# Performance work log

Measured on AMD Instinct MI355X. Metric: run time of the kernel, lower is better.

Reference implementation:

```python
import jax, jax.numpy as jnp
import numpy as np

B, N = 64, 32768

def setup_inputs() -> dict:
    key = jax.random.key(0)
    k1, k2, k3, k4 = jax.random.split(key, 4)
    audio = jax.random.normal(k1, (B, N), dtype=jnp.float32)
    g = jax.random.uniform(k2, (B, N, 1), dtype=jnp.float32)
    twoR = jax.random.uniform(k3, (B, N, 1), dtype=jnp.float32)
    mix = jax.random.uniform(k4, (B, N, 3), dtype=jnp.float32)
    return {"audio": audio, "g": g, "twoR": twoR, "mix": mix}


def _svf(audio, g, twoR, mix):
    b, n = audio.shape
    T = 1.0 / (1.0 + g * (g + twoR))                      # [B,N,1]
    ones = jnp.ones_like(g)
    # H: [B,N,2,2] time-varying state matrix
    H = T[..., None] * jnp.concatenate(
        [ones, -g, g, twoR * g + 1.0], axis=-1).reshape(b, n, 2, 2)
    gHB = (g * T) * jnp.concatenate([ones, g], axis=-1)   # [B,N,2]
    gHBx = gHB * audio[..., None]                          # [B,N,2]

    # Linear time-varying recurrence: Y_t = gHBx_t + H_t @ s_{t-1}; s_t = 2 Y_t - s_{t-1}
    def step(state, inp):
        Ht, ut = inp                                       # [B,2,2], [B,2]
        Yt = ut + jnp.einsum('bij,bj->bi', Ht, state)
        return 2.0 * Yt - state, Yt

    s0 = jnp.ones((b, 2), dtype=audio.dtype)
    _, Y = jax.lax.scan(step,
                        s0,
                        (jnp.moveaxis(H, 1, 0), jnp.moveaxis(gHBx, 1, 0)))
    Y = jnp.moveaxis(Y, 0, 1)                              # [B,N,2]

    twoR_ = twoR[..., 0]                                   # [B,N]
    y_bp, y_lp = Y[..., 0], Y[..., 1]
    y_hp = audio - twoR_ * y_bp - y_lp
    y_mixed = twoR_ * mix[..., 0] * y_bp + mix[..., 1] * y_lp + mix[..., 2] * y_hp
    return y_mixed


def reference(audio, g, twoR, mix):
    return _svf(audio, g, twoR, mix)
```

## Files before the change

### kernel.cpp

```cpp
#include <hip/hip_runtime.h>


#define BATCH     64
#define SEQ       32768
#define CHUNKS    16
#define CHUNK_LEN (SEQ / CHUNKS)
#define TPB       256
#define STEPS     (CHUNK_LEN / TPB)
#define NBLK      (BATCH * CHUNKS)

struct Aff { float a00, a01, a10, a11, b0, b1; };

__device__ __forceinline__ Aff compose(const Aff l, const Aff e) {
    Aff r;
    r.a00 = fmaf(l.a00, e.a00, l.a01 * e.a10);
    r.a01 = fmaf(l.a00, e.a01, l.a01 * e.a11);
    r.a10 = fmaf(l.a10, e.a00, l.a11 * e.a10);
    r.a11 = fmaf(l.a10, e.a01, l.a11 * e.a11);
    r.b0  = fmaf(l.a00, e.b0, fmaf(l.a01, e.b1, l.b0));
    r.b1  = fmaf(l.a10, e.b0, fmaf(l.a11, e.b1, l.b1));
    return r;
}

__device__ __forceinline__ Aff step_affine(float gi, float Ri, float xi) {
    float T  = 1.0f / fmaf(gi, gi + Ri, 1.0f);
    float Tg = T * gi;
    Aff r;
    r.a00 = 2.0f * T - 1.0f;
    r.a01 = -2.0f * Tg;
    r.a10 = 2.0f * Tg;
    r.a11 = 2.0f * fmaf(Tg, Ri, T) - 1.0f;
    r.b0  = 2.0f * Tg * xi;
    r.b1  = gi * r.b0;
    return r;
}

__device__ __forceinline__ Aff block_scan_incl(Aff v, Aff (*buf)[TPB], int t) {
    int src = 0;
    buf[0][t] = v;
    __syncthreads();
#pragma unroll
    for (int off = 1; off < TPB; off <<= 1) {
        Aff cur = buf[src][t];
        int idx = (t >= off) ? (t - off) : 0;
        Aff prev = buf[src][idx];
        Aff res = (t >= off) ? compose(cur, prev) : cur;
        buf[1 - src][t] = res;
        src ^= 1;
        __syncthreads();
    }
    return buf[src][t];
}

__device__ __forceinline__ void load8(const float* __restrict__ p, int base, float v[8]) {
    float4 a = *reinterpret_cast<const float4*>(p + base);
    float4 b = *reinterpret_cast<const float4*>(p + base + 4);
    v[0]=a.x; v[1]=a.y; v[2]=a.z; v[3]=a.w; v[4]=b.x; v[5]=b.y; v[6]=b.z; v[7]=b.w;
}

__global__ __launch_bounds__(TPB) void svf_chunk_reduce(
    const float* __restrict__ audio, const float* __restrict__ g,
    const float* __restrict__ twoR, Aff* __restrict__ chunk_comp)
{
    __shared__ Aff buf[2][TPB];
    const int t    = threadIdx.x;
    const int base = blockIdx.x * CHUNK_LEN + t * STEPS;

    float gv[STEPS], rv[STEPS], xv[STEPS];
    load8(g, base, gv); load8(twoR, base, rv); load8(audio, base, xv);

    Aff acc = step_affine(gv[0], rv[0], xv[0]);
#pragma unroll
    for (int i = 1; i < STEPS; ++i)
        acc = compose(step_affine(gv[i], rv[i], xv[i]), acc);

    Aff tot = block_scan_incl(acc, buf, t);
    if (t == TPB - 1) chunk_comp[blockIdx.x] = tot;
}

__global__ __launch_bounds__(TPB) void svf_emit(
    const float* __restrict__ audio, const float* __restrict__ g,
    const float* __restrict__ twoR, const float* __restrict__ mix,
    const Aff* __restrict__ chunk_comp, float* __restrict__ out)
{
    __shared__ Aff buf[2][TPB];
    const int blk  = blockIdx.x;
    const int b    = blk / CHUNKS;
    const int t    = threadIdx.x;
    const int base = blk * CHUNK_LEN + t * STEPS;

    float gv[STEPS], rv[STEPS], xv[STEPS];
    load8(g, base, gv); load8(twoR, base, rv); load8(audio, base, xv);

    Aff acc = step_affine(gv[0], rv[0], xv[0]);
#pragma unroll
    for (int i = 1; i < STEPS; ++i)
        acc = compose(step_affine(gv[i], rv[i], xv[i]), acc);

    Aff incl = block_scan_incl(acc, buf, t);
    buf[0][t] = incl;
    __syncthreads();

    float cs0 = 1.0f, cs1 = 1.0f;
    for (int cc = b * CHUNKS; cc < blk; ++cc) {
        Aff a = chunk_comp[cc];
        float n0 = fmaf(a.a00, cs0, fmaf(a.a01, cs1, a.b0));
        float n1 = fmaf(a.a10, cs0, fmaf(a.a11, cs1, a.b1));
        cs0 = n0; cs1 = n1;
    }

    float s0, s1;
    if (t == 0) { s0 = cs0; s1 = cs1; }
    else {
        Aff p = buf[0][t - 1];
        s0 = fmaf(p.a00, cs0, fmaf(p.a01, cs1, p.b0));
        s1 = fmaf(p.a10, cs0, fmaf(p.a11, cs1, p.b1));
    }

    const float4* m4 = reinterpret_cast<const float4*>(mix + 3 * base);
    float mv[24];
#pragma unroll
    for (int q = 0; q < 6; ++q) {
        float4 m = m4[q];
        mv[4*q+0]=m.x; mv[4*q+1]=m.y; mv[4*q+2]=m.z; mv[4*q+3]=m.w;
    }

    float ov[STEPS];
#pragma unroll
    for (int i = 0; i < STEPS; ++i) {
        float gi = gv[i], Ri = rv[i], xi = xv[i];
        float T  = 1.0f / fmaf(gi, gi + Ri, 1.0f);
        float w  = fmaf(gi, xi, s0);
        float Y0 = T * fmaf(-gi, s1, w);
        float Y1 = T * fmaf(gi, w, fmaf(Ri, gi, 1.0f) * s1);
        float hp = xi - Ri * Y0 - Y1;
        ov[i] = fmaf(Ri * mv[3*i], Y0, fmaf(mv[3*i+1], Y1, mv[3*i+2] * hp));
        s0 = fmaf(2.0f, Y0, -s0);
        s1 = fmaf(2.0f, Y1, -s1);
    }

    *reinterpret_cast<float4*>(out + base)     = make_float4(ov[0], ov[1], ov[2], ov[3]);
    *reinterpret_cast<float4*>(out + base + 4) = make_float4(ov[4], ov[5], ov[6], ov[7]);
}

extern "C" void kernel_launch(void* const* d_in, const int* in_sizes, int n_in,
                              void* d_out, int out_size, void* d_ws, size_t ws_size,
                              hipStream_t stream) {
    const float* audio = (const float*)d_in[0];
    const float* g     = (const float*)d_in[1];
    const float* twoR  = (const float*)d_in[2];
    const float* mix   = (const float*)d_in[3];
    float* out = (float*)d_out;
    Aff* chunk_comp = (Aff*)d_ws;

    svf_chunk_reduce<<<NBLK, TPB, 0, stream>>>(audio, g, twoR, chunk_comp);
    svf_emit<<<NBLK, TPB, 0, stream>>>(audio, g, twoR, mix, chunk_comp, out);
}
```

Baseline: 95.58 us.

## Fuse two-pass chunked scan into single kernel with decoupled flag-based chunk handoff

Merges the chunk-reduce and emit kernels into one kernel. Each block publishes its chunk affine composite through a global flag with release semantics, and later chunks spin on the flags of their predecessors. This removes the second full read of g, twoR and audio and one kernel launch. It adds a memset per call and relies on forward progress of earlier block indices for the spin-wait, which risks deadlock if blocks are not scheduled in order.

Result: slower. 157.4 us (+64.6%).

```diff
diff --git a/kernel.cpp b/kernel.cpp
--- a/kernel.cpp
+++ b/kernel.cpp
@@ -58,34 +58,19 @@
     v[0]=a.x; v[1]=a.y; v[2]=a.z; v[3]=a.w; v[4]=b.x; v[5]=b.y; v[6]=b.z; v[7]=b.w;
 }
 
-__global__ __launch_bounds__(TPB) void svf_chunk_reduce(
+__global__ __launch_bounds__(TPB, 4) void svf_fused(
     const float* __restrict__ audio, const float* __restrict__ g,
-    const float* __restrict__ twoR, Aff* __restrict__ chunk_comp)
+    const float* __restrict__ twoR, const float* __restrict__ mix,
+    float* __restrict__ out,
+    unsigned int* __restrict__ flags, Aff* __restrict__ chunk_aff)
 {
     __shared__ Aff buf[2][TPB];
-    const int t    = threadIdx.x;
-    const int base = blockIdx.x * CHUNK_LEN + t * STEPS;
+    __shared__ float pred[CHUNKS - 1][6];
+    __shared__ float cs_sh[2];
 
-    float gv[STEPS], rv[STEPS], xv[STEPS];
-    load8(g, base, gv); load8(twoR, base, rv); load8(audio, base, xv);
-
-    Aff acc = step_affine(gv[0], rv[0], xv[0]);
-#pragma unroll
-    for (int i = 1; i < STEPS; ++i)
-        acc = compose(step_affine(gv[i], rv[i], xv[i]), acc);
-
-    Aff tot = block_scan_incl(acc, buf, t);
-    if (t == TPB - 1) chunk_comp[blockIdx.x] = tot;
-}
-
-__global__ __launch_bounds__(TPB) void svf_emit(
-    const float* __restrict__ audio, const float* __restrict__ g,
-    const float* __restrict__ twoR, const float* __restrict__ mix,
-    const Aff* __restrict__ chunk_comp, float* __restrict__ out)
-{
-    __shared__ Aff buf[2][TPB];
     const int blk  = blockIdx.x;
-    const int b    = blk / CHUNKS;
+    const int b    = blk >> 4;
+    const int c    = blk & (CHUNKS - 1);
     const int t    = threadIdx.x;
     const int base = blk * CHUNK_LEN + t * STEPS;
 
@@ -97,17 +82,46 @@
     for (int i = 1; i < STEPS; ++i)
         acc = compose(step_affine(gv[i], rv[i], xv[i]), acc);
 
+    const float4* m4 = reinterpret_cast<const float4*>(mix + 3 * base);
+    float mv[24];
+#pragma unroll
+    for (int q = 0; q < 6; ++q) {
+        float4 m = m4[q];
+        mv[4*q+0]=m.x; mv[4*q+1]=m.y; mv[4*q+2]=m.z; mv[4*q+3]=m.w;
+    }
+
     Aff incl = block_scan_incl(acc, buf, t);
-    buf[0][t] = incl;
+
+    if (t == TPB - 1 && c < CHUNKS - 1) {
+        chunk_aff[blk] = incl;
+        __threadfence();
+        __hip_atomic_store(&flags[blk], 1u, __ATOMIC_RELEASE, __HIP_MEMORY_SCOPE_AGENT);
+    }
+
+    if (t < c) {
+        const int cc = b * CHUNKS + t;
+        while (__hip_atomic_load(&flags[cc], __ATOMIC_ACQUIRE,
+                                 __HIP_MEMORY_SCOPE_AGENT) == 0u) {
+            __builtin_amdgcn_s_sleep(1);
+        }
+        Aff a = chunk_aff[cc];
+        pred[t][0] = a.a00; pred[t][1] = a.a01; pred[t][2] = a.a10;
+        pred[t][3] = a.a11; pred[t][4] = a.b0;  pred[t][5] = a.b1;
+    }
     __syncthreads();
 
-    float cs0 = 1.0f, cs1 = 1.0f;
-    for (int cc = b * CHUNKS; cc < blk; ++cc) {
-        Aff a = chunk_comp[cc];
-        float n0 = fmaf(a.a00, cs0, fmaf(a.a01, cs1, a.b0));
-        float n1 = fmaf(a.a10, cs0, fmaf(a.a11, cs1, a.b1));
-        cs0 = n0; cs1 = n1;
+    if (t == 0) {
+        float s0 = 1.0f, s1 = 1.0f;
+        for (int j = 0; j < c; ++j) {
+            float n0 = fmaf(pred[j][0], s0, fmaf(pred[j][1], s1, pred[j][4]));
+            float n1 = fmaf(pred[j][2], s0, fmaf(pred[j][3], s1, pred[j][5]));
+            s0 = n0; s1 = n1;
+        }
+        cs_sh[0] = s0; cs_sh[1] = s1;
     }
+    __syncthreads();
+
+    const float cs0 = cs_sh[0], cs1 = cs_sh[1];
 
     float s0, s1;
     if (t == 0) { s0 = cs0; s1 = cs1; }
@@ -115,14 +129,6 @@
         Aff p = buf[0][t - 1];
         s0 = fmaf(p.a00, cs0, fmaf(p.a01, cs1, p.b0));
         s1 = fmaf(p.a10, cs0, fmaf(p.a11, cs1, p.b1));
-    }
-
-    const float4* m4 = reinterpret_cast<const float4*>(mix + 3 * base);
-    float mv[24];
-#pragma unroll
-    for (int q = 0; q < 6; ++q) {
-        float4 m = m4[q];
-        mv[4*q+0]=m.x; mv[4*q+1]=m.y; mv[4*q+2]=m.z; mv[4*q+3]=m.w;
     }
 
     float ov[STEPS];
@@ -151,8 +157,11 @@
     const float* twoR  = (const float*)d_in[2];
     const float* mix   = (const float*)d_in[3];
     float* out = (float*)d_out;
-    Aff* chunk_comp = (Aff*)d_ws;
 
-    svf_chunk_reduce<<<NBLK, TPB, 0, stream>>>(audio, g, twoR, chunk_comp);
-    svf_emit<<<NBLK, TPB, 0, stream>>>(audio, g, twoR, mix, chunk_comp, out);
+    unsigned int* flags = (unsigned int*)d_ws;
+    Aff* chunk_aff = (Aff*)((char*)d_ws + NBLK * sizeof(unsigned int));
+
+    hipMemsetAsync(flags, 0, NBLK * sizeof(unsigned int), stream);
+
+    svf_fused<<<NBLK, TPB, 0, stream>>>(audio, g, twoR, mix, out, flags, chunk_aff);
 }
```

## Fuse two-kernel chunked scan into single row-per-block kernel

Applied to the files above, without the earlier changes.

Replaces the two-pass chunked scan (a reduce kernel plus an emit kernel over 1024 blocks) with one kernel in which each block of 1024 threads handles a full row of 32768 samples. Each thread composes 32 steps, the block scans across threads, and the thread then re-reads its inputs to emit outputs. This removes the second launch, the workspace round trip and the serial cross-chunk carry loop. In exchange only 64 blocks run, which may underfill the GPU, and each thread's long per-element loop reads memory with a 128-byte stride between neighbouring threads, so accesses coalesce poorly.

Result: slower. 149.8 us (+56.7%).

```diff
diff --git a/kernel.cpp b/kernel.cpp
--- a/kernel.cpp
+++ b/kernel.cpp
@@ -1,13 +1,11 @@
 #include <hip/hip_runtime.h>
 
 
-#define BATCH     64
-#define SEQ       32768
-#define CHUNKS    16
-#define CHUNK_LEN (SEQ / CHUNKS)
-#define TPB       256
-#define STEPS     (CHUNK_LEN / TPB)
-#define NBLK      (BATCH * CHUNKS)
+#define BATCH 64
+#define SEQ   32768
+#define TPB   1024
+#define STEPS (SEQ / TPB)
+#define QUADS (STEPS / 4)
 
 struct Aff { float a00, a01, a10, a11, b0, b1; };
 
@@ -35,112 +33,79 @@
     return r;
 }
 
-__device__ __forceinline__ Aff block_scan_incl(Aff v, Aff (*buf)[TPB], int t) {
+__device__ __forceinline__ Aff quad_affine(float4 gq, float4 rq, float4 xq) {
+    Aff a = step_affine(gq.x, rq.x, xq.x);
+    a = compose(step_affine(gq.y, rq.y, xq.y), a);
+    a = compose(step_affine(gq.z, rq.z, xq.z), a);
+    a = compose(step_affine(gq.w, rq.w, xq.w), a);
+    return a;
+}
+
+__device__ __forceinline__ float emit1(float gi, float Ri, float xi,
+                                       float m0, float m1, float m2,
+                                       float& s0, float& s1) {
+    float T  = 1.0f / fmaf(gi, gi + Ri, 1.0f);
+    float w  = fmaf(gi, xi, s0);
+    float Y0 = T * fmaf(-gi, s1, w);
+    float Y1 = T * fmaf(gi, w, fmaf(Ri, gi, 1.0f) * s1);
+    float hp = xi - Ri * Y0 - Y1;
+    float o  = fmaf(Ri * m0, Y0, fmaf(m1, Y1, m2 * hp));
+    s0 = fmaf(2.0f, Y0, -s0);
+    s1 = fmaf(2.0f, Y1, -s1);
+    return o;
+}
+
+__global__ __launch_bounds__(TPB, 4) void svf_row(
+    const float* __restrict__ audio, const float* __restrict__ g,
+    const float* __restrict__ twoR, const float* __restrict__ mix,
+    float* __restrict__ out)
+{
+    __shared__ Aff buf[2][TPB];
+    const int t    = threadIdx.x;
+    const int base = blockIdx.x * SEQ + t * STEPS;
+
+    const float4* g4 = reinterpret_cast<const float4*>(g + base);
+    const float4* r4 = reinterpret_cast<const float4*>(twoR + base);
+    const float4* x4 = reinterpret_cast<const float4*>(audio + base);
+
+    Aff acc = quad_affine(g4[0], r4[0], x4[0]);
+#pragma unroll 2
+    for (int q = 1; q < QUADS; ++q)
+        acc = compose(quad_affine(g4[q], r4[q], x4[q]), acc);
+
     int src = 0;
-    buf[0][t] = v;
+    buf[0][t] = acc;
     __syncthreads();
 #pragma unroll
     for (int off = 1; off < TPB; off <<= 1) {
-        Aff cur = buf[src][t];
-        int idx = (t >= off) ? (t - off) : 0;
-        Aff prev = buf[src][idx];
-        Aff res = (t >= off) ? compose(cur, prev) : cur;
-        buf[1 - src][t] = res;
+        Aff prev = buf[src][(t >= off) ? (t - off) : 0];
+        if (t >= off) acc = compose(acc, prev);
+        buf[1 - src][t] = acc;
         src ^= 1;
         __syncthreads();
     }
-    return buf[src][t];
-}
-
-__device__ __forceinline__ void load8(const float* __restrict__ p, int base, float v[8]) {
-    float4 a = *reinterpret_cast<const float4*>(p + base);
-    float4 b = *reinterpret_cast<const float4*>(p + base + 4);
-    v[0]=a.x; v[1]=a.y; v[2]=a.z; v[3]=a.w; v[4]=b.x; v[5]=b.y; v[6]=b.z; v[7]=b.w;
-}
-
-__global__ __launch_bounds__(TPB) void svf_chunk_reduce(
-    const float* __restrict__ audio, const float* __restrict__ g,
-    const float* __restrict__ twoR, Aff* __restrict__ chunk_comp)
-{
-    __shared__ Aff buf[2][TPB];
-    const int t    = threadIdx.x;
-    const int base = blockIdx.x * CHUNK_LEN + t * STEPS;
-
-    float gv[STEPS], rv[STEPS], xv[STEPS];
-    load8(g, base, gv); load8(twoR, base, rv); load8(audio, base, xv);
-
-    Aff acc = step_affine(gv[0], rv[0], xv[0]);
-#pragma unroll
-    for (int i = 1; i < STEPS; ++i)
-        acc = compose(step_affine(gv[i], rv[i], xv[i]), acc);
-
-    Aff tot = block_scan_incl(acc, buf, t);
-    if (t == TPB - 1) chunk_comp[blockIdx.x] = tot;
-}
-
-__global__ __launch_bounds__(TPB) void svf_emit(
-    const float* __restrict__ audio, const float* __restrict__ g,
-    const float* __restrict__ twoR, const float* __restrict__ mix,
-    const Aff* __restrict__ chunk_comp, float* __restrict__ out)
-{
-    __shared__ Aff buf[2][TPB];
-    const int blk  = blockIdx.x;
-    const int b    = blk / CHUNKS;
-    const int t    = threadIdx.x;
-    const int base = blk * CHUNK_LEN + t * STEPS;
-
-    float gv[STEPS], rv[STEPS], xv[STEPS];
-    load8(g, base, gv); load8(twoR, base, rv); load8(audio, base, xv);
-
-    Aff acc = step_affine(gv[0], rv[0], xv[0]);
-#pragma unroll
-    for (int i = 1; i < STEPS; ++i)
-        acc = compose(step_affine(gv[i], rv[i], xv[i]), acc);
-
-    Aff incl = block_scan_incl(acc, buf, t);
-    buf[0][t] = incl;
-    __syncthreads();
-
-    float cs0 = 1.0f, cs1 = 1.0f;
-    for (int cc = b * CHUNKS; cc < blk; ++cc) {
-        Aff a = chunk_comp[cc];
-        float n0 = fmaf(a.a00, cs0, fmaf(a.a01, cs1, a.b0));
-        float n1 = fmaf(a.a10, cs0, fmaf(a.a11, cs1, a.b1));
-        cs0 = n0; cs1 = n1;
-    }
 
     float s0, s1;
-    if (t == 0) { s0 = cs0; s1 = cs1; }
+    if (t == 0) { s0 = 1.0f; s1 = 1.0f; }
     else {
         Aff p = buf[0][t - 1];
-        s0 = fmaf(p.a00, cs0, fmaf(p.a01, cs1, p.b0));
-        s1 = fmaf(p.a10, cs0, fmaf(p.a11, cs1, p.b1));
+        s0 = p.a00 + p.a01 + p.b0;
+        s1 = p.a10 + p.a11 + p.b1;
     }
 
     const float4* m4 = reinterpret_cast<const float4*>(mix + 3 * base);
-    float mv[24];
-#pragma unroll
-    for (int q = 0; q < 6; ++q) {
-        float4 m = m4[q];
-        mv[4*q+0]=m.x; mv[4*q+1]=m.y; mv[4*q+2]=m.z; mv[4*q+3]=m.w;
+    float4* o4 = reinterpret_cast<float4*>(out + base);
+#pragma unroll 1
+    for (int q = 0; q < QUADS; ++q) {
+        float4 gq = g4[q], rq = r4[q], xq = x4[q];
+        float4 ma = m4[3*q+0], mb = m4[3*q+1], mc = m4[3*q+2];
+        float4 ov;
+        ov.x = emit1(gq.x, rq.x, xq.x, ma.x, ma.y, ma.z, s0, s1);
+        ov.y = emit1(gq.y, rq.y, xq.y, ma.w, mb.x, mb.y, s0, s1);
+        ov.z = emit1(gq.z, rq.z, xq.z, mb.z, mb.w, mc.x, s0, s1);
+        ov.w = emit1(gq.w, rq.w, xq.w, mc.y, mc.z, mc.w, s0, s1);
+        o4[q] = ov;
     }
-
-    float ov[STEPS];
-#pragma unroll
-    for (int i = 0; i < STEPS; ++i) {
-        float gi = gv[i], Ri = rv[i], xi = xv[i];
-        float T  = 1.0f / fmaf(gi, gi + Ri, 1.0f);
-        float w  = fmaf(gi, xi, s0);
-        float Y0 = T * fmaf(-gi, s1, w);
-        float Y1 = T * fmaf(gi, w, fmaf(Ri, gi, 1.0f) * s1);
-        float hp = xi - Ri * Y0 - Y1;
-        ov[i] = fmaf(Ri * mv[3*i], Y0, fmaf(mv[3*i+1], Y1, mv[3*i+2] * hp));
-        s0 = fmaf(2.0f, Y0, -s0);
-        s1 = fmaf(2.0f, Y1, -s1);
-    }
-
-    *reinterpret_cast<float4*>(out + base)     = make_float4(ov[0], ov[1], ov[2], ov[3]);
-    *reinterpret_cast<float4*>(out + base + 4) = make_float4(ov[4], ov[5], ov[6], ov[7]);
 }
 
 extern "C" void kernel_launch(void* const* d_in, const int* in_sizes, int n_in,
@@ -151,8 +116,7 @@
     const float* twoR  = (const float*)d_in[2];
     const float* mix   = (const float*)d_in[3];
     float* out = (float*)d_out;
-    Aff* chunk_comp = (Aff*)d_ws;
+    (void)d_ws; (void)ws_size;
 
-    svf_chunk_reduce<<<NBLK, TPB, 0, stream>>>(audio, g, twoR, chunk_comp);
-    svf_emit<<<NBLK, TPB, 0, stream>>>(audio, g, twoR, mix, chunk_comp, out);
+    svf_row<<<BATCH, TPB, 0, stream>>>(audio, g, twoR, mix, out);
 }
```

## Store per-thread prefixes in reduce kernel and use wave-shuffle scan

Applied to the files above, without the earlier changes.

The block scan moves from a shared-memory Hillis-Steele scan with a barrier per step to a 64-lane shuffle scan, followed by a small cross-wave combine through shared memory. The first kernel now writes every thread's inclusive prefix to workspace. The emit kernel reads that prefix instead of recomputing the per-thread affine composition and block scan, so it no longer needs a second scan or its barriers. The cost is 32 extra bytes per thread written and read back through global memory, and the workspace must be large enough to hold them.

Result: no change. 97.37 us (+1.9%).

```diff
diff --git a/kernel.cpp b/kernel.cpp
--- a/kernel.cpp
+++ b/kernel.cpp
@@ -35,21 +35,15 @@
     return r;
 }
 
-__device__ __forceinline__ Aff block_scan_incl(Aff v, Aff (*buf)[TPB], int t) {
-    int src = 0;
-    buf[0][t] = v;
-    __syncthreads();
-#pragma unroll
-    for (int off = 1; off < TPB; off <<= 1) {
-        Aff cur = buf[src][t];
-        int idx = (t >= off) ? (t - off) : 0;
-        Aff prev = buf[src][idx];
-        Aff res = (t >= off) ? compose(cur, prev) : cur;
-        buf[1 - src][t] = res;
-        src ^= 1;
-        __syncthreads();
-    }
-    return buf[src][t];
+__device__ __forceinline__ Aff shfl_up_aff(const Aff v, int delta) {
+    Aff r;
+    r.a00 = __shfl_up(v.a00, delta, 64);
+    r.a01 = __shfl_up(v.a01, delta, 64);
+    r.a10 = __shfl_up(v.a10, delta, 64);
+    r.a11 = __shfl_up(v.a11, delta, 64);
+    r.b0  = __shfl_up(v.b0,  delta, 64);
+    r.b1  = __shfl_up(v.b1,  delta, 64);
+    return r;
 }
 
 __device__ __forceinline__ void load8(const float* __restrict__ p, int base, float v[8]) {
@@ -58,35 +52,18 @@
     v[0]=a.x; v[1]=a.y; v[2]=a.z; v[3]=a.w; v[4]=b.x; v[5]=b.y; v[6]=b.z; v[7]=b.w;
 }
 
-__global__ __launch_bounds__(TPB) void svf_chunk_reduce(
+__global__ __launch_bounds__(TPB, 4) void svf_reduce(
     const float* __restrict__ audio, const float* __restrict__ g,
-    const float* __restrict__ twoR, Aff* __restrict__ chunk_comp)
+    const float* __restrict__ twoR,
+    float4* __restrict__ pref,
+    float4* __restrict__ chunk_comp)
 {
-    __shared__ Aff buf[2][TPB];
+    __shared__ Aff wtot[TPB / 64];
+
+    const int blk  = blockIdx.x;
     const int t    = threadIdx.x;
-    const int base = blockIdx.x * CHUNK_LEN + t * STEPS;
-
-    float gv[STEPS], rv[STEPS], xv[STEPS];
-    load8(g, base, gv); load8(twoR, base, rv); load8(audio, base, xv);
-
-    Aff acc = step_affine(gv[0], rv[0], xv[0]);
-#pragma unroll
-    for (int i = 1; i < STEPS; ++i)
-        acc = compose(step_affine(gv[i], rv[i], xv[i]), acc);
-
-    Aff tot = block_scan_incl(acc, buf, t);
-    if (t == TPB - 1) chunk_comp[blockIdx.x] = tot;
-}
-
-__global__ __launch_bounds__(TPB) void svf_emit(
-    const float* __restrict__ audio, const float* __restrict__ g,
-    const float* __restrict__ twoR, const float* __restrict__ mix,
-    const Aff* __restrict__ chunk_comp, float* __restrict__ out)
-{
-    __shared__ Aff buf[2][TPB];
-    const int blk  = blockIdx.x;
-    const int b    = blk / CHUNKS;
-    const int t    = threadIdx.x;
+    const int lane = t & 63;
+    const int wv   = t >> 6;
     const int base = blk * CHUNK_LEN + t * STEPS;
 
     float gv[STEPS], rv[STEPS], xv[STEPS];
@@ -97,25 +74,50 @@
     for (int i = 1; i < STEPS; ++i)
         acc = compose(step_affine(gv[i], rv[i], xv[i]), acc);
 
-    Aff incl = block_scan_incl(acc, buf, t);
-    buf[0][t] = incl;
-    __syncthreads();
-
-    float cs0 = 1.0f, cs1 = 1.0f;
-    for (int cc = b * CHUNKS; cc < blk; ++cc) {
-        Aff a = chunk_comp[cc];
-        float n0 = fmaf(a.a00, cs0, fmaf(a.a01, cs1, a.b0));
-        float n1 = fmaf(a.a10, cs0, fmaf(a.a11, cs1, a.b1));
-        cs0 = n0; cs1 = n1;
+#pragma unroll
+    for (int off = 1; off < 64; off <<= 1) {
+        Aff p = shfl_up_aff(acc, off);
+        if (lane >= off) acc = compose(acc, p);
     }
 
-    float s0, s1;
-    if (t == 0) { s0 = cs0; s1 = cs1; }
-    else {
-        Aff p = buf[0][t - 1];
-        s0 = fmaf(p.a00, cs0, fmaf(p.a01, cs1, p.b0));
-        s1 = fmaf(p.a10, cs0, fmaf(p.a11, cs1, p.b1));
+    if (lane == 63) wtot[wv] = acc;
+    __syncthreads();
+    if (wv > 0) {
+        Aff wp = wtot[0];
+        for (int j = 1; j < wv; ++j) wp = compose(wtot[j], wp);
+        acc = compose(acc, wp);
     }
+
+    const int idx = blk * TPB + t;
+    pref[2 * idx]     = make_float4(acc.a00, acc.a01, acc.a10, acc.a11);
+    pref[2 * idx + 1] = make_float4(acc.b0,  acc.b1,  0.0f,    0.0f);
+
+    if (t == TPB - 1) {
+        chunk_comp[2 * blk]     = make_float4(acc.a00, acc.a01, acc.a10, acc.a11);
+        chunk_comp[2 * blk + 1] = make_float4(acc.b0,  acc.b1,  0.0f,    0.0f);
+    }
+}
+
+__global__ __launch_bounds__(TPB, 4) void svf_emit(
+    const float* __restrict__ audio, const float* __restrict__ g,
+    const float* __restrict__ twoR, const float* __restrict__ mix,
+    const float4* __restrict__ pref, const float4* __restrict__ chunk_comp,
+    float* __restrict__ out)
+{
+    const int blk  = blockIdx.x;
+    const int b    = blk >> 4;
+    const int t    = threadIdx.x;
+    const int base = blk * CHUNK_LEN + t * STEPS;
+
+    float4 pA, pB;
+    if (t > 0) {
+        const int pidx = blk * TPB + t - 1;
+        pA = pref[2 * pidx];
+        pB = pref[2 * pidx + 1];
+    }
+
+    float gv[STEPS], rv[STEPS], xv[STEPS];
+    load8(g, base, gv); load8(twoR, base, rv); load8(audio, base, xv);
 
     const float4* m4 = reinterpret_cast<const float4*>(mix + 3 * base);
     float mv[24];
@@ -123,6 +125,22 @@
     for (int q = 0; q < 6; ++q) {
         float4 m = m4[q];
         mv[4*q+0]=m.x; mv[4*q+1]=m.y; mv[4*q+2]=m.z; mv[4*q+3]=m.w;
+    }
+
+    float cs0 = 1.0f, cs1 = 1.0f;
+    for (int cc = b * CHUNKS; cc < blk; ++cc) {
+        float4 A  = chunk_comp[2 * cc];
+        float4 Bv = chunk_comp[2 * cc + 1];
+        float n0 = fmaf(A.x, cs0, fmaf(A.y, cs1, Bv.x));
+        float n1 = fmaf(A.z, cs0, fmaf(A.w, cs1, Bv.y));
+        cs0 = n0; cs1 = n1;
+    }
+
+    float s0, s1;
+    if (t == 0) { s0 = cs0; s1 = cs1; }
+    else {
+        s0 = fmaf(pA.x, cs0, fmaf(pA.y, cs1, pB.x));
+        s1 = fmaf(pA.z, cs0, fmaf(pA.w, cs1, pB.y));
     }
 
     float ov[STEPS];
@@ -151,8 +169,10 @@
     const float* twoR  = (const float*)d_in[2];
     const float* mix   = (const float*)d_in[3];
     float* out = (float*)d_out;
-    Aff* chunk_comp = (Aff*)d_ws;
 
-    svf_chunk_reduce<<<NBLK, TPB, 0, stream>>>(audio, g, twoR, chunk_comp);
-    svf_emit<<<NBLK, TPB, 0, stream>>>(audio, g, twoR, mix, chunk_comp, out);
+    float4* pref       = (float4*)d_ws;
+    float4* chunk_comp = (float4*)((char*)d_ws + (size_t)NBLK * TPB * 32);
+
+    svf_reduce<<<NBLK, TPB, 0, stream>>>(audio, g, twoR, pref, chunk_comp);
+    svf_emit<<<NBLK, TPB, 0, stream>>>(audio, g, twoR, mix, pref, chunk_comp, out);
 }
```
